# Performance work log

Hardware: AMD Instinct MI355X
Metric: run time of the kernel (lower is better)

## Reference

```python
import jax, jax.numpy as jnp
import numpy as np

H = 12            # num_heads
GRID = 14         # sqrt(num_patches)
NP_ = GRID * GRID # num_patches = 196


def _relative_position_index():
    coords = np.stack(np.meshgrid(np.arange(GRID), np.arange(GRID), indexing='ij'))  # [2,14,14]
    flat = coords.reshape(2, -1)                                   # [2,196]
    rel = flat[:, :, None] - flat[:, None, :]                      # [2,196,196]
    rel = rel.transpose(1, 2, 0).astype(np.int32)                  # [196,196,2]
    rel[..., 0] += GRID - 1
    rel[..., 1] += GRID - 1
    rel[..., 0] *= 2 * GRID - 1
    return rel.sum(-1)                                             # [196,196] in [0,729)


def setup_inputs() -> dict:
    key = jax.random.key(0)
    k1, k2, k3, k4 = jax.random.split(key, 4)
    B, N, C = 64, NP_ + 1, 768
    return {
        'x': jax.random.normal(k1, (B, N, C), dtype=jnp.float32),
        'w_qkv': jax.random.normal(k2, (3 * C, C), dtype=jnp.float32) * 0.02,
        'w_proj': jax.random.normal(k3, (C, C), dtype=jnp.float32) * 0.02,
        'b_proj': jnp.zeros((C,), dtype=jnp.float32),
        # torch inits the table to zeros; use small randn so the bias path is exercised
        'rpb_table': jax.random.normal(k4, ((2 * GRID - 1) ** 2, H), dtype=jnp.float32) * 0.02,
        'rel_idx': jnp.asarray(_relative_position_index()),
    }


def reference(x, w_qkv, w_proj, b_proj, rpb_table, rel_idx):
    B, N, C = x.shape
    hd = C // H
    scale = hd ** -0.5
    qkv = (x @ w_qkv.T).reshape(B, N, 3, H, hd).transpose(2, 0, 3, 1, 4)  # [3,B,H,N,hd]
    q, k, v = qkv[0] * scale, qkv[1], qkv[2]
    attn = jnp.einsum('bhqd,bhkd->bhqk', q, k)                            # [B,H,N,N]
    bias = rpb_table[rel_idx.reshape(-1)].reshape(NP_, NP_, H).transpose(2, 0, 1)  # [H,196,196]
    attn = attn.at[:, :, 1:, 1:].add(bias[None])                          # skip CLS row/col
    attn = jax.nn.softmax(attn, axis=-1)
    out = jnp.einsum('bhqk,bhkd->bqhd', attn, v).reshape(B, N, C)
    return out @ w_proj.T + b_proj
```

## Files before the change

kernel.cpp:

```cpp
#include <hip/hip_runtime.h>

typedef float f32x4 __attribute__((ext_vector_type(4)));
typedef short short8 __attribute__((ext_vector_type(8)));

#define DEVI static __device__ __forceinline__

DEVI ushort f2bf(float f) {
  unsigned u = __builtin_bit_cast(unsigned, f);
  u += 0x7fffu + ((u >> 16) & 1u);
  return (ushort)(u >> 16);
}

DEVI short8 pack8(float4 a, float4 b) {
  union { ushort u[8]; short8 v; } t;
  t.u[0] = f2bf(a.x); t.u[1] = f2bf(a.y); t.u[2] = f2bf(a.z); t.u[3] = f2bf(a.w);
  t.u[4] = f2bf(b.x); t.u[5] = f2bf(b.y); t.u[6] = f2bf(b.z); t.u[7] = f2bf(b.w);
  return t.v;
}

DEVI f32x4 MFMA16(short8 a, short8 b, f32x4 c) {
  return __builtin_amdgcn_mfma_f32_16x16x32_bf16(a, b, c, 0, 0, 0);
}

DEVI void gld16(const ushort* g, ushort* l) {
  __builtin_amdgcn_global_load_lds(
      (const __attribute__((address_space(1))) unsigned int*)g,
      (__attribute__((address_space(3))) unsigned int*)l, 16, 0, 0);
}

__global__ void cvt_bf16(const float* __restrict__ s, ushort* __restrict__ d, int n8) {
  int i = blockIdx.x * 256 + threadIdx.x;
  if (i >= n8) return;
  float4 a = ((const float4*)s)[i * 2];
  float4 b = ((const float4*)s)[i * 2 + 1];
  ((short8*)d)[i] = pack8(a, b);
}

__global__ void prep_bias(const float* __restrict__ table, const int* __restrict__ rel_idx,
                          float* __restrict__ bias) {
  int i = blockIdx.x * 256 + threadIdx.x;
  if (i >= 12 * 208 * 208) return;
  int k = i % 208;
  int t = i / 208;
  int q = t % 208;
  int h = t / 208;
  float v;
  if (k >= 197) v = -1e30f;
  else if (q == 0 || k == 0 || q >= 197) v = 0.0f;
  else v = table[rel_idx[(q - 1) * 196 + (k - 1)] * 12 + h];
  bias[i] = v;
}

template <int MODE, int NBN>
__launch_bounds__(256, 4)
__global__ void gemm128(const ushort* __restrict__ A, const ushort* __restrict__ B,
                        ushort* __restrict__ q, ushort* __restrict__ k,
                        ushort* __restrict__ v,
                        const float* __restrict__ bprj, float* __restrict__ out) {
  __shared__ __align__(16) ushort As[2][4096];
  __shared__ __align__(16) ushort Bs[2][4096];

  const int tid = threadIdx.x;
  const int lane = tid & 63, wid = tid >> 6;
  const int wm = wid >> 1, wn = wid & 1;
  const int l15 = lane & 15, l4 = lane >> 4;

  const int nwg = gridDim.x;
  const int qc = nwg >> 3, rc = nwg & 7;
  const int xcd = blockIdx.x & 7, sub = blockIdx.x >> 3;
  const int wgid = (xcd < rc ? xcd * (qc + 1) : rc * (qc + 1) + (xcd - rc) * qc) + sub;
  const int bn = wgid % NBN, bm = wgid / NBN;

  const int c0 = wid * 2, c1 = wid * 2 + 1;
  const int r0 = c0 * 16 + (lane >> 2);
  const int r1 = c1 * 16 + (lane >> 2);
  const int g = lane & 3;
  const int col0 = (g << 3) ^ ((r0 & 6) << 2);
  const int col1 = (g << 3) ^ ((r1 & 6) << 2);
  long ar0 = bm * 128 + r0; if (ar0 > 12607) ar0 = 12607;
  long ar1 = bm * 128 + r1; if (ar1 > 12607) ar1 = 12607;
  const ushort* pA0 = A + ar0 * 768 + col0;
  const ushort* pA1 = A + ar1 * 768 + col1;
  const ushort* pB0 = B + (size_t)(bn * 128 + r0) * 768 + col0;
  const ushort* pB1 = B + (size_t)(bn * 128 + r1) * 768 + col1;

  const int xk = (l4 * 8) ^ ((l15 & 6) << 2);
  int aoff[4], boff[4];
#pragma unroll
  for (int m = 0; m < 4; m++) aoff[m] = (wm * 64 + m * 16 + l15) * 32 + xk;
#pragma unroll
  for (int n = 0; n < 4; n++) boff[n] = (wn * 64 + n * 16 + l15) * 32 + xk;

  f32x4 acc[4][4];
#pragma unroll
  for (int m = 0; m < 4; m++)
#pragma unroll
    for (int n = 0; n < 4; n++) acc[m][n] = (f32x4)0.0f;

#define STAGE(BUF, KO)                          \
  gld16(pA0 + (KO), &As[BUF][c0 * 512]);        \
  gld16(pA1 + (KO), &As[BUF][c1 * 512]);        \
  gld16(pB0 + (KO), &Bs[BUF][c0 * 512]);        \
  gld16(pB1 + (KO), &Bs[BUF][c1 * 512]);

#define COMPUTE(BUF)                                                \
  {                                                                 \
    short8 af[4], bv[4];                                            \
    _Pragma("unroll") for (int m = 0; m < 4; m++)                   \
        af[m] = *(const short8*)&As[BUF][aoff[m]];                  \
    _Pragma("unroll") for (int n = 0; n < 4; n++)                   \
        bv[n] = *(const short8*)&Bs[BUF][boff[n]];                  \
    __builtin_amdgcn_s_setprio(1);                                  \
    _Pragma("unroll") for (int m = 0; m < 4; m++)                   \
        _Pragma("unroll") for (int n = 0; n < 4; n++)               \
            acc[m][n] = MFMA16(af[m], bv[n], acc[m][n]);            \
    __builtin_amdgcn_s_setprio(0);                                  \
  }

  STAGE(0, 0)
  for (int t = 0; t < 23; ++t) {
    asm volatile("s_waitcnt vmcnt(0) lgkmcnt(0)" ::: "memory");
    __builtin_amdgcn_s_barrier();
    __builtin_amdgcn_sched_barrier(0);
    STAGE((t + 1) & 1, (t + 1) * 32)
    COMPUTE(t & 1)
  }
  asm volatile("s_waitcnt vmcnt(0) lgkmcnt(0)" ::: "memory");
  __builtin_amdgcn_s_barrier();
  __builtin_amdgcn_sched_barrier(0);
  COMPUTE(1)

  if (MODE == 0) {
    const int s = bn / 6;
    ushort* dst = (s == 0) ? q : ((s == 1) ? k : v);
    const float qs = (s == 0) ? 0.125f : 1.0f;
    const int cbase = bn * 128 + wn * 64 - s * 768;
    const int hh = cbase >> 6;
#pragma unroll
    for (int m = 0; m < 4; m++) {
#pragma unroll
      for (int r = 0; r < 4; r++) {
        int gm = bm * 128 + wm * 64 + m * 16 + l4 * 4 + r;
        if (gm >= 12608) continue;
        int b = gm / 197;
        int ns = gm - b * 197;
        size_t base = (size_t)((b * 12 + hh) * 197 + ns) * 64;
#pragma unroll
        for (int n = 0; n < 4; n++)
          dst[base + n * 16 + l15] = f2bf(acc[m][n][r] * qs);
      }
    }
  } else {
    float bb[4];
#pragma unroll
    for (int n = 0; n < 4; n++) bb[n] = bprj[bn * 128 + wn * 64 + n * 16 + l15];
#pragma unroll
    for (int m = 0; m < 4; m++) {
#pragma unroll
      for (int r = 0; r < 4; r++) {
        int gm = bm * 128 + wm * 64 + m * 16 + l4 * 4 + r;
        if (gm >= 12608) continue;
#pragma unroll
        for (int n = 0; n < 4; n++)
          out[(size_t)gm * 768 + bn * 128 + wn * 64 + n * 16 + l15] = acc[m][n][r] + bb[n];
      }
    }
  }
#undef STAGE
#undef COMPUTE
}

__launch_bounds__(512)
__global__ void attn(const ushort* __restrict__ qws, const ushort* __restrict__ kws,
                     const ushort* __restrict__ vws, const float* __restrict__ biasws,
                     ushort* __restrict__ aout) {
  __shared__ __align__(16) ushort Ks[208 * 72];
  __shared__ __align__(16) ushort Vt[64 * 232];
  __shared__ __align__(16) ushort Ps[8 * 16 * 232];

  const int bh = blockIdx.x;
  const int b = bh / 12;
  const int h = bh - b * 12;
  const ushort* qb = qws + (size_t)bh * 197 * 64;
  const ushort* kb = kws + (size_t)bh * 197 * 64;
  const ushort* vb = vws + (size_t)bh * 197 * 64;

  const int tid = threadIdx.x;
  const int lane = tid & 63, wid = tid >> 6;
  const int l15 = lane & 15, l4 = lane >> 4;

  for (int c = tid; c < 208 * 8; c += 512) {
    int n = c >> 3, col = (c & 7) << 3;
    short8 v = (short8)0;
    if (n < 197) v = *(const short8*)(kb + n * 64 + col);
    *(short8*)&Ks[n * 72 + col] = v;
  }
  for (int c = tid; c < 224 * 8; c += 512) {
    int n = c % 224;
    int d0 = (c / 224) << 3;
    ushort tmp[8] = {0, 0, 0, 0, 0, 0, 0, 0};
    if (n < 197) {
      short8 v = *(const short8*)(vb + n * 64 + d0);
#pragma unroll
      for (int j = 0; j < 8; j++) tmp[j] = (ushort)v[j];
    }
#pragma unroll
    for (int j = 0; j < 8; j++) Vt[(d0 + j) * 232 + n] = tmp[j];
  }
  __syncthreads();

  ushort* pb = &Ps[wid * (16 * 232)];
  const float* biasb = biasws + (size_t)h * 208 * 208;

  for (int t = wid; t < 13; t += 8) {
    const int q0 = t * 16;
    int qr = q0 + l15; if (qr > 196) qr = 196;
    short8 aq0 = *(const short8*)(qb + qr * 64 + (l4 << 3));
    short8 aq1 = *(const short8*)(qb + qr * 64 + 32 + (l4 << 3));

    f32x4 sc[13];
    __builtin_amdgcn_s_setprio(1);
#pragma unroll
    for (int ct = 0; ct < 13; ct++) {
      short8 b0 = *(const short8*)&Ks[(ct * 16 + l15) * 72 + (l4 << 3)];
      short8 b1 = *(const short8*)&Ks[(ct * 16 + l15) * 72 + 32 + (l4 << 3)];
      f32x4 s = (f32x4)0.0f;
      s = MFMA16(aq0, b0, s);
      s = MFMA16(aq1, b1, s);
      sc[ct] = s;
    }
    __builtin_amdgcn_s_setprio(0);

    float mx[4] = {-1e38f, -1e38f, -1e38f, -1e38f};
#pragma unroll
    for (int ct = 0; ct < 13; ct++) {
#pragma unroll
      for (int r = 0; r < 4; r++) {
        float bv = biasb[(q0 + l4 * 4 + r) * 208 + ct * 16 + l15];
        float v = sc[ct][r] + bv;
        sc[ct][r] = v;
        mx[r] = fmaxf(mx[r], v);
      }
    }
#pragma unroll
    for (int r = 0; r < 4; r++) {
      mx[r] = fmaxf(mx[r], __shfl_xor(mx[r], 1));
      mx[r] = fmaxf(mx[r], __shfl_xor(mx[r], 2));
      mx[r] = fmaxf(mx[r], __shfl_xor(mx[r], 4));
      mx[r] = fmaxf(mx[r], __shfl_xor(mx[r], 8));
    }
    float sum[4] = {0.f, 0.f, 0.f, 0.f};
#pragma unroll
    for (int ct = 0; ct < 13; ct++) {
#pragma unroll
      for (int r = 0; r < 4; r++) {
        float p = __expf(sc[ct][r] - mx[r]);
        sc[ct][r] = p;
        sum[r] += p;
      }
    }
#pragma unroll
    for (int r = 0; r < 4; r++) {
      sum[r] += __shfl_xor(sum[r], 1);
      sum[r] += __shfl_xor(sum[r], 2);
      sum[r] += __shfl_xor(sum[r], 4);
      sum[r] += __shfl_xor(sum[r], 8);
    }

#pragma unroll
    for (int ct = 0; ct < 13; ct++)
#pragma unroll
      for (int r = 0; r < 4; r++)
        pb[(l4 * 4 + r) * 232 + ct * 16 + l15] = f2bf(sc[ct][r]);
#pragma unroll
    for (int r = 0; r < 4; r++)
      pb[(l4 * 4 + r) * 232 + 208 + l15] = 0;

    short8 pa[7];
#pragma unroll
    for (int kk = 0; kk < 7; kk++)
      pa[kk] = *(const short8*)&pb[l15 * 232 + kk * 32 + (l4 << 3)];
    f32x4 o[4];
    __builtin_amdgcn_s_setprio(1);
#pragma unroll
    for (int dt = 0; dt < 4; dt++) {
      f32x4 acc = (f32x4)0.0f;
#pragma unroll
      for (int kk = 0; kk < 7; kk++) {
        short8 bv = *(const short8*)&Vt[(dt * 16 + l15) * 232 + kk * 32 + (l4 << 3)];
        acc = MFMA16(pa[kk], bv, acc);
      }
      o[dt] = acc;
    }
    __builtin_amdgcn_s_setprio(0);

    float rs[4];
#pragma unroll
    for (int r = 0; r < 4; r++) rs[r] = 1.0f / sum[r];
#pragma unroll
    for (int dt = 0; dt < 4; dt++) {
#pragma unroll
      for (int r = 0; r < 4; r++) {
        int row = q0 + l4 * 4 + r;
        if (row < 197) {
          float v = o[dt][r] * rs[r];
          aout[(size_t)(b * 197 + row) * 768 + h * 64 + dt * 16 + l15] = f2bf(v);
        }
      }
    }
  }
}

extern "C" void kernel_launch(void* const* d_in, const int* in_sizes, int n_in,
                              void* d_out, int out_size, void* d_ws, size_t ws_size,
                              hipStream_t stream) {
  const float* x      = (const float*)d_in[0];
  const float* w_qkv  = (const float*)d_in[1];
  const float* w_proj = (const float*)d_in[2];
  const float* b_proj = (const float*)d_in[3];
  const float* rpb    = (const float*)d_in[4];
  const int*   relidx = (const int*)d_in[5];
  float* out = (float*)d_out;

  char* ws = (char*)d_ws;
  const size_t HB = (size_t)12608 * 768 * 2;
  ushort* xbf   = (ushort*)(ws);
  ushort* qws   = (ushort*)(ws + HB);
  ushort* kws   = (ushort*)(ws + 2 * HB);
  ushort* vws   = (ushort*)(ws + 3 * HB);
  float*  bias  = (float*)(ws + 4 * HB);
  ushort* wqkvb = (ushort*)(ws + 4 * HB + 2076672);
  ushort* wprjb = (ushort*)(ws + 4 * HB + 2076672 + 3538944);
  ushort* aout  = xbf;

  hipLaunchKernelGGL(prep_bias, dim3((12 * 208 * 208 + 255) / 256), dim3(256), 0, stream,
                     rpb, relidx, bias);
  hipLaunchKernelGGL(cvt_bf16, dim3((12608 * 768 / 8 + 255) / 256), dim3(256), 0, stream,
                     x, xbf, 12608 * 768 / 8);
  hipLaunchKernelGGL(cvt_bf16, dim3((2304 * 768 / 8 + 255) / 256), dim3(256), 0, stream,
                     w_qkv, wqkvb, 2304 * 768 / 8);
  hipLaunchKernelGGL(cvt_bf16, dim3((768 * 768 / 8 + 255) / 256), dim3(256), 0, stream,
                     w_proj, wprjb, 768 * 768 / 8);
  hipLaunchKernelGGL((gemm128<0, 18>), dim3(18 * 99), dim3(256), 0, stream,
                     xbf, wqkvb, qws, kws, vws, nullptr, nullptr);
  hipLaunchKernelGGL(attn, dim3(768), dim3(512), 0, stream, qws, kws, vws, bias, aout);
  hipLaunchKernelGGL((gemm128<1, 6>), dim3(6 * 99), dim3(256), 0, stream,
                     aout, wprjb, nullptr, nullptr, nullptr, b_proj, out);
}
```

Baseline: 145.7 us.

## Triple-buffer GEMM k-loop with partial vmcnt waits and fuse prep kernels

The bf16 GEMM mainloop moves from double to triple buffering in LDS. Loads are issued two stages ahead, and waits use vmcnt(4) so one stage's loads stay in flight during compute. The launch bound drops to 3 blocks per CU to fit the larger LDS footprint. Separately, the bias preparation and three fp32-to-bf16 conversions are merged into a single block-partitioned kernel to cut launch overhead. Lower occupancy may offset the deeper pipelining.

```diff
diff --git a/kernel.cpp b/kernel.cpp
--- a/kernel.cpp
+++ b/kernel.cpp
@@ -28,37 +28,49 @@
       (__attribute__((address_space(3))) unsigned int*)l, 16, 0, 0);
 }
 
-__global__ void cvt_bf16(const float* __restrict__ s, ushort* __restrict__ d, int n8) {
-  int i = blockIdx.x * 256 + threadIdx.x;
-  if (i >= n8) return;
-  float4 a = ((const float4*)s)[i * 2];
-  float4 b = ((const float4*)s)[i * 2 + 1];
-  ((short8*)d)[i] = pack8(a, b);
-}
-
-__global__ void prep_bias(const float* __restrict__ table, const int* __restrict__ rel_idx,
-                          float* __restrict__ bias) {
-  int i = blockIdx.x * 256 + threadIdx.x;
-  if (i >= 12 * 208 * 208) return;
-  int k = i % 208;
-  int t = i / 208;
-  int q = t % 208;
-  int h = t / 208;
-  float v;
-  if (k >= 197) v = -1e30f;
-  else if (q == 0 || k == 0 || q >= 197) v = 0.0f;
-  else v = table[rel_idx[(q - 1) * 196 + (k - 1)] * 12 + h];
-  bias[i] = v;
+__global__ void prep_all(const float* __restrict__ table, const int* __restrict__ rel_idx,
+                         float* __restrict__ bias,
+                         const float* __restrict__ x, ushort* __restrict__ xbf,
+                         const float* __restrict__ wq, ushort* __restrict__ wqb,
+                         const float* __restrict__ wp, ushort* __restrict__ wpb) {
+  const int bid = blockIdx.x, tid = threadIdx.x;
+  if (bid < 2028) {
+    int i = bid * 256 + tid;
+    int k = i % 208;
+    int t = i / 208;
+    int q = t % 208;
+    int h = t / 208;
+    float v;
+    if (k >= 197) v = -1e30f;
+    else if (q == 0 || k == 0 || q >= 197) v = 0.0f;
+    else v = table[rel_idx[(q - 1) * 196 + (k - 1)] * 12 + h];
+    bias[i] = v;
+  } else if (bid < 6756) {
+    int i = (bid - 2028) * 256 + tid;
+    float4 a = ((const float4*)x)[i * 2];
+    float4 b = ((const float4*)x)[i * 2 + 1];
+    ((short8*)xbf)[i] = pack8(a, b);
+  } else if (bid < 7620) {
+    int i = (bid - 6756) * 256 + tid;
+    float4 a = ((const float4*)wq)[i * 2];
+    float4 b = ((const float4*)wq)[i * 2 + 1];
+    ((short8*)wqb)[i] = pack8(a, b);
+  } else {
+    int i = (bid - 7620) * 256 + tid;
+    float4 a = ((const float4*)wp)[i * 2];
+    float4 b = ((const float4*)wp)[i * 2 + 1];
+    ((short8*)wpb)[i] = pack8(a, b);
+  }
 }
 
 template <int MODE, int NBN>
-__launch_bounds__(256, 4)
+__launch_bounds__(256, 3)
 __global__ void gemm128(const ushort* __restrict__ A, const ushort* __restrict__ B,
                         ushort* __restrict__ q, ushort* __restrict__ k,
                         ushort* __restrict__ v,
                         const float* __restrict__ bprj, float* __restrict__ out) {
-  __shared__ __align__(16) ushort As[2][4096];
-  __shared__ __align__(16) ushort Bs[2][4096];
+  __shared__ __align__(16) ushort As[3][4096];
+  __shared__ __align__(16) ushort Bs[3][4096];
 
   const int tid = threadIdx.x;
   const int lane = tid & 63, wid = tid >> 6;
@@ -97,19 +109,19 @@
 #pragma unroll
     for (int n = 0; n < 4; n++) acc[m][n] = (f32x4)0.0f;
 
-#define STAGE(BUF, KO)                          \
-  gld16(pA0 + (KO), &As[BUF][c0 * 512]);        \
-  gld16(pA1 + (KO), &As[BUF][c1 * 512]);        \
-  gld16(pB0 + (KO), &Bs[BUF][c0 * 512]);        \
-  gld16(pB1 + (KO), &Bs[BUF][c1 * 512]);
-
-#define COMPUTE(BUF)                                                \
+#define STAGE(SL, KO)                           \
+  gld16(pA0 + (KO), &As[SL][c0 * 512]);         \
+  gld16(pA1 + (KO), &As[SL][c1 * 512]);         \
+  gld16(pB0 + (KO), &Bs[SL][c0 * 512]);         \
+  gld16(pB1 + (KO), &Bs[SL][c1 * 512]);
+
+#define COMPUTE(SL)                                                 \
   {                                                                 \
     short8 af[4], bv[4];                                            \
     _Pragma("unroll") for (int m = 0; m < 4; m++)                   \
-        af[m] = *(const short8*)&As[BUF][aoff[m]];                  \
+        af[m] = *(const short8*)&As[SL][aoff[m]];                   \
     _Pragma("unroll") for (int n = 0; n < 4; n++)                   \
-        bv[n] = *(const short8*)&Bs[BUF][boff[n]];                  \
+        bv[n] = *(const short8*)&Bs[SL][boff[n]];                   \
     __builtin_amdgcn_s_setprio(1);                                  \
     _Pragma("unroll") for (int m = 0; m < 4; m++)                   \
         _Pragma("unroll") for (int n = 0; n < 4; n++)               \
@@ -118,17 +130,29 @@
   }
 
   STAGE(0, 0)
-  for (int t = 0; t < 23; ++t) {
-    asm volatile("s_waitcnt vmcnt(0) lgkmcnt(0)" ::: "memory");
+  STAGE(1, 32)
+
+  int sl_c = 0, sl_s = 2;
+  for (int t = 0; t < 22; ++t) {
+    asm volatile("s_waitcnt vmcnt(4)" ::: "memory");
+    asm volatile("s_waitcnt lgkmcnt(0)" ::: "memory");
     __builtin_amdgcn_s_barrier();
     __builtin_amdgcn_sched_barrier(0);
-    STAGE((t + 1) & 1, (t + 1) * 32)
-    COMPUTE(t & 1)
-  }
-  asm volatile("s_waitcnt vmcnt(0) lgkmcnt(0)" ::: "memory");
+    STAGE(sl_s, (t + 2) * 32)
+    COMPUTE(sl_c)
+    sl_c = (sl_c == 2) ? 0 : sl_c + 1;
+    sl_s = (sl_s == 2) ? 0 : sl_s + 1;
+  }
+  asm volatile("s_waitcnt vmcnt(4)" ::: "memory");
+  asm volatile("s_waitcnt lgkmcnt(0)" ::: "memory");
   __builtin_amdgcn_s_barrier();
   __builtin_amdgcn_sched_barrier(0);
   COMPUTE(1)
+  asm volatile("s_waitcnt vmcnt(0)" ::: "memory");
+  asm volatile("s_waitcnt lgkmcnt(0)" ::: "memory");
+  __builtin_amdgcn_s_barrier();
+  __builtin_amdgcn_sched_barrier(0);
+  COMPUTE(2)
 
   if (MODE == 0) {
     const int s = bn / 6;
@@ -333,14 +357,8 @@
   ushort* wprjb = (ushort*)(ws + 4 * HB + 2076672 + 3538944);
   ushort* aout  = xbf;
 
-  hipLaunchKernelGGL(prep_bias, dim3((12 * 208 * 208 + 255) / 256), dim3(256), 0, stream,
-                     rpb, relidx, bias);
-  hipLaunchKernelGGL(cvt_bf16, dim3((12608 * 768 / 8 + 255) / 256), dim3(256), 0, stream,
-                     x, xbf, 12608 * 768 / 8);
-  hipLaunchKernelGGL(cvt_bf16, dim3((2304 * 768 / 8 + 255) / 256), dim3(256), 0, stream,
-                     w_qkv, wqkvb, 2304 * 768 / 8);
-  hipLaunchKernelGGL(cvt_bf16, dim3((768 * 768 / 8 + 255) / 256), dim3(256), 0, stream,
-                     w_proj, wprjb, 768 * 768 / 8);
+  hipLaunchKernelGGL(prep_all, dim3(7908), dim3(256), 0, stream,
+                     rpb, relidx, bias, x, xbf, w_qkv, wqkvb, w_proj, wprjb);
   hipLaunchKernelGGL((gemm128<0, 18>), dim3(18 * 99), dim3(256), 0, stream,
                      xbf, wqkvb, qws, kws, vws, nullptr, nullptr);
   hipLaunchKernelGGL(attn, dim3(768), dim3(512), 0, stream, qws, kws, vws, bias, aout);
```

After: 145.1 us. Within noise of the previous version (-0.4%).
